# Performance work log

Measured on AMD Instinct MI355X. Metric: run time of the kernel, lower is better.

Reference implementation:

```python
import jax, jax.numpy as jnp
import numpy as np

NUM_ITEM = 2000
DIM_KEY = 256
DIM_VALUE = 128  # number of memory slots
B, T = 256, 512


def setup_inputs() -> dict:
    key = jax.random.key(0)
    ks = jax.random.split(key, 16)
    s = 0.05
    return {
        'item_seq': jax.random.randint(ks[0], (B, T), 0, NUM_ITEM),
        'correct_seq': jax.random.randint(ks[1], (B, T), 0, 2),
        'k_emb': jax.random.normal(ks[2], (NUM_ITEM, DIM_KEY)) * s,
        'v_emb': jax.random.normal(ks[3], (2 * NUM_ITEM, DIM_KEY)) * s,
        'Mk': jax.random.normal(ks[4], (DIM_VALUE, DIM_KEY)) * s,
        'Mv0': jax.random.normal(ks[5], (DIM_VALUE, DIM_KEY)) * s,
        'e_W': jax.random.normal(ks[6], (DIM_KEY, DIM_KEY)) * s,
        'e_b': jnp.zeros((DIM_KEY,)),
        'a_W': jax.random.normal(ks[7], (DIM_KEY, DIM_KEY)) * s,
        'a_b': jnp.zeros((DIM_KEY,)),
        'f_W': jax.random.normal(ks[8], (DIM_KEY, 2 * DIM_KEY)) * s,
        'f_b': jnp.zeros((DIM_KEY,)),
        'p_W': jax.random.normal(ks[9], (1, DIM_KEY)) * s,
        'p_b': jnp.zeros((1,)),
    }


def reference(item_seq, correct_seq, k_emb, v_emb, Mk, Mv0, e_W, e_b, a_W, a_b, f_W, f_b, p_W, p_b):
    num_item = k_emb.shape[0]
    x = item_seq + num_item * correct_seq            # [B, T]
    k = k_emb[item_seq]                              # [B, T, dk]
    v = v_emb[x]                                     # [B, T, dk]
    w = jax.nn.softmax(jnp.einsum('btk,vk->btv', k, Mk), axis=-1)  # [B, T, dv]
    e = jax.nn.sigmoid(v @ e_W.T + e_b)              # erase gate   [B, T, dk]
    a = jnp.tanh(v @ a_W.T + a_b)                    # add vector   [B, T, dk]

    bsz = item_seq.shape[0]
    Mvt0 = jnp.broadcast_to(Mv0[None], (bsz,) + Mv0.shape)  # [B, dv, dk]

    def step(Mvt, inp):
        wt, et, at = inp                              # [B,dv], [B,dk], [B,dk]
        # read uses the memory state BEFORE the update (Mv[:, :-1] in torch)
        read = jnp.einsum('bv,bvk->bk', wt, Mvt)      # [B, dk]
        wt_ = wt[:, :, None]
        Mvt = Mvt * (1.0 - wt_ * et[:, None, :]) + wt_ * at[:, None, :]
        return Mvt, read

    # time-major scan; Mvt stays resident in the carry
    _, reads = jax.lax.scan(
        step, Mvt0,
        (jnp.swapaxes(w, 0, 1), jnp.swapaxes(e, 0, 1), jnp.swapaxes(a, 0, 1)))
    reads = jnp.swapaxes(reads, 0, 1)                 # [B, T, dk]

    f = jnp.tanh(jnp.concatenate([reads, k], axis=-1) @ f_W.T + f_b)  # [B, T, dk]
    # dropout is identity in eval mode
    predict_score = jax.nn.sigmoid(f @ p_W.T + p_b)[..., 0]          # [B, T]
    return predict_score
```

## Files before the change

### kernel.cpp

```cpp
#include <hip/hip_runtime.h>
#include <hip/hip_bf16.h>


#define T_SEQ 512
#define DK    256
#define DV    128
#define NITEM 2000
#define BT    131072

typedef __attribute__((ext_vector_type(8))) short bf16x8;
typedef __attribute__((ext_vector_type(4))) float f32x4;
typedef __attribute__((ext_vector_type(2))) float f32x2;

__device__ __forceinline__ float bf2f(unsigned short u) {
    return __uint_as_float(((unsigned int)u) << 16);
}
__device__ __forceinline__ unsigned short f2bf(float x) {
    unsigned int u = __float_as_uint(x);
    return (unsigned short)((u + 0x7fffu + ((u >> 16) & 1u)) >> 16);
}
__device__ __forceinline__ float fast_rcp(float x) { return __builtin_amdgcn_rcpf(x); }
__device__ __forceinline__ float fast_sigmoid(float x) { return fast_rcp(1.f + __expf(-x)); }
__device__ __forceinline__ float fast_tanh(float x) {
    float t = __expf(2.f * x);
    return (t - 1.f) * fast_rcp(t + 1.f);
}

__device__ __forceinline__ f32x2 pk_fma(f32x2 a, f32x2 b, f32x2 c) {
#if __has_builtin(__builtin_elementwise_fma)
    return __builtin_elementwise_fma(a, b, c);
#else
    f32x2 d; d.x = fmaf(a.x, b.x, c.x); d.y = fmaf(a.y, b.y, c.y); return d;
#endif
}

__global__ __launch_bounds__(256) void k0_cvt(
    const float* __restrict__ s0, const float* __restrict__ s1,
    const float* __restrict__ s2, const float* __restrict__ s3,
    const float* __restrict__ s4,
    unsigned short* __restrict__ d0, unsigned short* __restrict__ d1,
    unsigned short* __restrict__ d2, unsigned short* __restrict__ d3,
    unsigned short* __restrict__ d4,
    int n0, int n1, int n2, int n3, int n4)
{
    const float* s; unsigned short* d; int n;
    switch (blockIdx.y) {
        case 0:  s = s0; d = d0; n = n0; break;
        case 1:  s = s1; d = d1; n = n1; break;
        case 2:  s = s2; d = d2; n = n2; break;
        case 3:  s = s3; d = d3; n = n3; break;
        default: s = s4; d = d4; n = n4; break;
    }
    int i4 = (blockIdx.x * 256 + threadIdx.x) * 4;
    if (i4 < n) {
        float4 v = *(const float4*)(s + i4);
        ushort4 o;
        o.x = f2bf(v.x); o.y = f2bf(v.y); o.z = f2bf(v.z); o.w = f2bf(v.w);
        *(ushort4*)(d + i4) = o;
    }
}

__global__ __launch_bounds__(256) void k1_wea(
    const int* __restrict__ item_seq, const int* __restrict__ correct_seq,
    const unsigned short* __restrict__ k_bf, const unsigned short* __restrict__ v_bf,
    const unsigned short* __restrict__ Mk_bf,
    const unsigned short* __restrict__ eW_bf, const float* __restrict__ e_b,
    const unsigned short* __restrict__ aW_bf, const float* __restrict__ a_b,
    unsigned short* __restrict__ Wout, unsigned short* __restrict__ Eout,
    unsigned short* __restrict__ Aout)
{
    const int m_tile = blockIdx.x;
    const int n_tile = blockIdx.y;
    const int tid  = threadIdx.x;
    const int lane = tid & 63;
    const int wv   = tid >> 6;

    __shared__ int idx_s[128];
    __shared__ unsigned short A_s[128 * 40];
    __shared__ unsigned short B_s[128 * 40];

    const unsigned short* Atab = (n_tile == 0) ? k_bf : v_bf;
    const unsigned short* Wtab; int wrow0;
    if (n_tile == 0)      { Wtab = Mk_bf; wrow0 = 0;   }
    else if (n_tile == 1) { Wtab = eW_bf; wrow0 = 0;   }
    else if (n_tile == 2) { Wtab = eW_bf; wrow0 = 128; }
    else if (n_tile == 3) { Wtab = aW_bf; wrow0 = 0;   }
    else                  { Wtab = aW_bf; wrow0 = 128; }

    if (tid < 128) {
        int pos = m_tile * 128 + tid;
        int it = item_seq[pos];
        int co = correct_seq[pos];
        idx_s[tid] = (n_tile == 0) ? it : (it + NITEM * co);
    }
    __syncthreads();

    int myrow[4], myc4[4], myidx[4];
    #pragma unroll
    for (int j = 0; j < 4; ++j) {
        int chunk = tid + 256 * j;
        myrow[j] = chunk >> 3;
        myc4[j]  = chunk & 7;
        myidx[j] = idx_s[myrow[j]];
    }

    f32x4 acc[2][8];
    #pragma unroll
    for (int mi = 0; mi < 2; ++mi)
        #pragma unroll
        for (int ni = 0; ni < 8; ++ni)
            acc[mi][ni] = (f32x4){0.f, 0.f, 0.f, 0.f};

    for (int bk = 0; bk < 8; ++bk) {
        int k0 = bk * 32;
        #pragma unroll
        for (int j = 0; j < 4; ++j) {
            int row = myrow[j], c4 = myc4[j];
            *(ushort4*)&A_s[row * 40 + c4 * 4] =
                *(const ushort4*)(Atab + (long)myidx[j] * DK + k0 + c4 * 4);
            *(ushort4*)&B_s[row * 40 + c4 * 4] =
                *(const ushort4*)(Wtab + (long)(wrow0 + row) * DK + k0 + c4 * 4);
        }
        __syncthreads();

        const int kq = lane >> 4;
        const int rr = lane & 15;
        bf16x8 af[2], bfr[8];
        #pragma unroll
        for (int mi = 0; mi < 2; ++mi)
            af[mi] = *(const bf16x8*)&A_s[(wv * 32 + mi * 16 + rr) * 40 + kq * 8];
        #pragma unroll
        for (int ni = 0; ni < 8; ++ni)
            bfr[ni] = *(const bf16x8*)&B_s[(ni * 16 + rr) * 40 + kq * 8];
        #pragma unroll
        for (int ni = 0; ni < 8; ++ni)
            #pragma unroll
            for (int mi = 0; mi < 2; ++mi)
                acc[mi][ni] = __builtin_amdgcn_mfma_f32_16x16x32_bf16(
                    af[mi], bfr[ni], acc[mi][ni], 0, 0, 0);
        __syncthreads();
    }

    const int rowbase = m_tile * 128 + wv * 32;
    const int cgrp = lane >> 4;
    const int cc   = lane & 15;

    if (n_tile == 0) {
        #pragma unroll
        for (int mi = 0; mi < 2; ++mi) {
            #pragma unroll
            for (int i = 0; i < 4; ++i) {
                float m = -1e30f;
                #pragma unroll
                for (int ni = 0; ni < 8; ++ni) m = fmaxf(m, acc[mi][ni][i]);
                m = fmaxf(m, __shfl_xor(m, 1));
                m = fmaxf(m, __shfl_xor(m, 2));
                m = fmaxf(m, __shfl_xor(m, 4));
                m = fmaxf(m, __shfl_xor(m, 8));
                float p[8]; float s = 0.f;
                #pragma unroll
                for (int ni = 0; ni < 8; ++ni) { p[ni] = __expf(acc[mi][ni][i] - m); s += p[ni]; }
                s += __shfl_xor(s, 1); s += __shfl_xor(s, 2);
                s += __shfl_xor(s, 4); s += __shfl_xor(s, 8);
                float inv = fast_rcp(s);
                int row = rowbase + mi * 16 + cgrp * 4 + i;
                #pragma unroll
                for (int ni = 0; ni < 8; ++ni)
                    Wout[(long)row * 128 + ni * 16 + cc] = f2bf(p[ni] * inv);
            }
        }
    } else {
        const bool is_e = (n_tile <= 2);
        const float* bias = is_e ? e_b : a_b;
        const int colbase = (is_e ? (n_tile - 1) : (n_tile - 3)) * 128;
        unsigned short* Out = is_e ? Eout : Aout;
        #pragma unroll
        for (int ni = 0; ni < 8; ++ni) {
            int colp = colbase + ni * 16 + cc;
            float bb = bias[colp];
            #pragma unroll
            for (int mi = 0; mi < 2; ++mi) {
                #pragma unroll
                for (int i = 0; i < 4; ++i) {
                    int row = rowbase + mi * 16 + cgrp * 4 + i;
                    float x = acc[mi][ni][i] + bb;
                    float v = is_e ? fast_sigmoid(x) : fast_tanh(x);
                    Out[(long)row * 256 + colp] = f2bf(v);
                }
            }
        }
    }
}

__global__ __launch_bounds__(512, 1) void k2_scan(
    const float* __restrict__ Mv0,
    const unsigned short* __restrict__ Wws, const unsigned short* __restrict__ Ews,
    const unsigned short* __restrict__ Aws, unsigned short* __restrict__ Rws)
{
    const int b   = blockIdx.x;
    const int tid = threadIdx.x;
    const int kq  = tid & 63;
    const int vo  = tid >> 6;

    __shared__ float4 part[8][8][64];

    f32x2 Ma[16], Mb[16];
    #pragma unroll
    for (int j = 0; j < 16; ++j) {
        float4 m4 = *(const float4*)(Mv0 + (vo * 16 + j) * DK + kq * 4);
        Ma[j] = (f32x2){m4.x, m4.y};
        Mb[j] = (f32x2){m4.z, m4.w};
    }

    const long pos0 = (long)b * T_SEQ;
    const unsigned int* Wd = (const unsigned int*)Wws;
    const int wslot = vo * 8 + (kq & 7);

    unsigned int wdA = Wd[(pos0 + 0) * 64 + wslot];
    uint2 edA = *(const uint2*)(Ews + (pos0 + 0) * 256 + kq * 4);
    uint2 adA = *(const uint2*)(Aws + (pos0 + 0) * 256 + kq * 4);
    unsigned int wdB = Wd[(pos0 + 1) * 64 + wslot];
    uint2 edB = *(const uint2*)(Ews + (pos0 + 1) * 256 + kq * 4);
    uint2 adB = *(const uint2*)(Aws + (pos0 + 1) * 256 + kq * 4);

#define K2_STEP(T, SLOT, WD, ED, AD)                                           \
    {                                                                          \
        const unsigned int wd = WD;                                            \
        const uint2 ed = ED, ad = AD;                                          \
        {         \
            long pn = pos0 + ((T) + 2 < T_SEQ ? (T) + 2 : T_SEQ - 1);          \
            WD = Wd[pn * 64 + wslot];                                          \
            ED = *(const uint2*)(Ews + pn * 256 + kq * 4);                     \
            AD = *(const uint2*)(Aws + pn * 256 + kq * 4);                     \
        }                                                                      \
        f32x2 ea = (f32x2){__uint_as_float(ed.x << 16),                        \
                           __uint_as_float(ed.x & 0xffff0000u)};               \
        f32x2 eb = (f32x2){__uint_as_float(ed.y << 16),                        \
                           __uint_as_float(ed.y & 0xffff0000u)};               \
        f32x2 aa = (f32x2){__uint_as_float(ad.x << 16),                        \
                           __uint_as_float(ad.x & 0xffff0000u)};               \
        f32x2 ab = (f32x2){__uint_as_float(ad.y << 16),                        \
                           __uint_as_float(ad.y & 0xffff0000u)};               \
        f32x2 nea = -ea, neb = -eb;                                            \
        f32x2 ra = (f32x2){0.f, 0.f}, rb = (f32x2){0.f, 0.f};                  \
        _Pragma("unroll")                                                      \
        for (int p = 0; p < 8; ++p) {                                          \
            unsigned int d = __builtin_amdgcn_readlane(wd, p);                 \
            float s0 = __uint_as_float(d << 16);                               \
            float s1 = __uint_as_float(d & 0xffff0000u);                       \
            {                                                                  \
                f32x2 s2 = (f32x2){s0, s0};                                    \
                f32x2 ma = Ma[2 * p], mb = Mb[2 * p];                          \
                ra = pk_fma(s2, ma, ra);                                       \
                rb = pk_fma(s2, mb, rb);                                       \
                f32x2 ta = pk_fma(nea, ma, aa);                                \
                f32x2 tb = pk_fma(neb, mb, ab);                                \
                Ma[2 * p] = pk_fma(s2, ta, ma);                                \
                Mb[2 * p] = pk_fma(s2, tb, mb);                                \
            }                                                                  \
            {                                                                  \
                f32x2 s2 = (f32x2){s1, s1};                                    \
                f32x2 ma = Ma[2 * p + 1], mb = Mb[2 * p + 1];                  \
                ra = pk_fma(s2, ma, ra);                                       \
                rb = pk_fma(s2, mb, rb);                                       \
                f32x2 ta = pk_fma(nea, ma, aa);                                \
                f32x2 tb = pk_fma(neb, mb, ab);                                \
                Ma[2 * p + 1] = pk_fma(s2, ta, ma);                            \
                Mb[2 * p + 1] = pk_fma(s2, tb, mb);                            \
            }                                                                  \
        }                                                                      \
        part[SLOT][vo][kq] = float4{ra.x, ra.y, rb.x, rb.y};                   \
    }

    for (int tc = 0; tc < T_SEQ; tc += 8) {
        K2_STEP(tc + 0, 0, wdA, edA, adA)
        K2_STEP(tc + 1, 1, wdB, edB, adB)
        K2_STEP(tc + 2, 2, wdA, edA, adA)
        K2_STEP(tc + 3, 3, wdB, edB, adB)
        K2_STEP(tc + 4, 4, wdA, edA, adA)
        K2_STEP(tc + 5, 5, wdB, edB, adB)
        K2_STEP(tc + 6, 6, wdA, edA, adA)
        K2_STEP(tc + 7, 7, wdB, edB, adB)
        __syncthreads();
        {
            float4 s = part[vo][0][kq];
            #pragma unroll
            for (int w2 = 1; w2 < 8; ++w2) {
                float4 r = part[vo][w2][kq];
                s.x += r.x; s.y += r.y; s.z += r.z; s.w += r.w;
            }
            ushort4 o;
            o.x = f2bf(s.x); o.y = f2bf(s.y); o.z = f2bf(s.z); o.w = f2bf(s.w);
            *(ushort4*)(Rws + (pos0 + tc + vo) * 256 + kq * 4) = o;
        }
        __syncthreads();
    }
#undef K2_STEP
}

__global__ __launch_bounds__(256) void k3_f(
    const int* __restrict__ item_seq,
    const unsigned short* __restrict__ k_bf,
    const unsigned short* __restrict__ fW_bf, const float* __restrict__ f_b,
    const unsigned short* __restrict__ Rws,
    unsigned short* __restrict__ Fout)
{
    const int m_tile = blockIdx.x;
    const int nt  = blockIdx.y;
    const int tid = threadIdx.x;
    const int lane = tid & 63;
    const int wv   = tid >> 6;

    __shared__ int idx_s[128];
    __shared__ unsigned short A_s[128 * 40];
    __shared__ unsigned short B_s[128 * 40];

    if (tid < 128) idx_s[tid] = item_seq[m_tile * 128 + tid];
    __syncthreads();

    int myrow[4], myc4[4], myidx[4];
    #pragma unroll
    for (int j = 0; j < 4; ++j) {
        int chunk = tid + 256 * j;
        myrow[j] = chunk >> 3;
        myc4[j]  = chunk & 7;
        myidx[j] = idx_s[myrow[j]];
    }

    f32x4 acc[2][8];
    #pragma unroll
    for (int mi = 0; mi < 2; ++mi)
        #pragma unroll
        for (int ni = 0; ni < 8; ++ni)
            acc[mi][ni] = (f32x4){0.f, 0.f, 0.f, 0.f};

    for (int bk = 0; bk < 16; ++bk) {
        int k0 = bk * 32;
        #pragma unroll
        for (int j = 0; j < 4; ++j) {
            int row = myrow[j], c4 = myc4[j];
            ushort4 ap;
            if (k0 < 256) {
                long pos = (long)m_tile * 128 + row;
                ap = *(const ushort4*)(Rws + pos * 256 + k0 + c4 * 4);
            } else {
                ap = *(const ushort4*)(k_bf + (long)myidx[j] * DK + (k0 - 256) + c4 * 4);
            }
            *(ushort4*)&A_s[row * 40 + c4 * 4] = ap;
            *(ushort4*)&B_s[row * 40 + c4 * 4] =
                *(const ushort4*)(fW_bf + (long)(nt * 128 + row) * 512 + k0 + c4 * 4);
        }
        __syncthreads();

        const int kq = lane >> 4;
        const int rr = lane & 15;
        bf16x8 af[2], bfr[8];
        #pragma unroll
        for (int mi = 0; mi < 2; ++mi)
            af[mi] = *(const bf16x8*)&A_s[(wv * 32 + mi * 16 + rr) * 40 + kq * 8];
        #pragma unroll
        for (int ni = 0; ni < 8; ++ni)
            bfr[ni] = *(const bf16x8*)&B_s[(ni * 16 + rr) * 40 + kq * 8];
        #pragma unroll
        for (int ni = 0; ni < 8; ++ni)
            #pragma unroll
            for (int mi = 0; mi < 2; ++mi)
                acc[mi][ni] = __builtin_amdgcn_mfma_f32_16x16x32_bf16(
                    af[mi], bfr[ni], acc[mi][ni], 0, 0, 0);
        __syncthreads();
    }

    const int rowbase = m_tile * 128 + wv * 32;
    const int cgrp = lane >> 4;
    const int cc   = lane & 15;
    #pragma unroll
    for (int ni = 0; ni < 8; ++ni) {
        int colp = nt * 128 + ni * 16 + cc;
        float bb = f_b[colp];
        #pragma unroll
        for (int mi = 0; mi < 2; ++mi) {
            #pragma unroll
            for (int i = 0; i < 4; ++i) {
                int row = rowbase + mi * 16 + cgrp * 4 + i;
                Fout[(long)row * 256 + colp] = f2bf(fast_tanh(acc[mi][ni][i] + bb));
            }
        }
    }
}

__global__ __launch_bounds__(256) void k4_pred(
    const unsigned short* __restrict__ Fws,
    const float* __restrict__ p_W, const float* __restrict__ p_b,
    float* __restrict__ out)
{
    const int tid  = threadIdx.x;
    const int lane = tid & 63;
    const int wgid = blockIdx.x * 4 + (tid >> 6);
    const float4 pw = *(const float4*)(p_W + lane * 4);
    const float pb = p_b[0];
    #pragma unroll 4
    for (int r = 0; r < 64; ++r) {
        long row = (long)wgid * 64 + r;
        ushort4 q = *(const ushort4*)(Fws + row * 256 + lane * 4);
        float partial = bf2f(q.x) * pw.x + bf2f(q.y) * pw.y
                      + bf2f(q.z) * pw.z + bf2f(q.w) * pw.w;
        #pragma unroll
        for (int off = 32; off >= 1; off >>= 1) partial += __shfl_xor(partial, off);
        if (lane == 0) out[row] = fast_sigmoid(partial + pb);
    }
}

extern "C" void kernel_launch(void* const* d_in, const int* in_sizes, int n_in,
                              void* d_out, int out_size, void* d_ws, size_t ws_size,
                              hipStream_t stream)
{
    const int*   item_seq    = (const int*)d_in[0];
    const int*   correct_seq = (const int*)d_in[1];
    const float* k_emb = (const float*)d_in[2];
    const float* v_emb = (const float*)d_in[3];
    const float* Mk    = (const float*)d_in[4];
    const float* Mv0   = (const float*)d_in[5];
    const float* e_W   = (const float*)d_in[6];
    const float* e_b   = (const float*)d_in[7];
    const float* a_W   = (const float*)d_in[8];
    const float* a_b   = (const float*)d_in[9];
    const float* f_W   = (const float*)d_in[10];
    const float* f_b   = (const float*)d_in[11];
    const float* p_W   = (const float*)d_in[12];
    const float* p_b   = (const float*)d_in[13];
    float* out = (float*)d_out;

    char* ws = (char*)d_ws;
    unsigned short* Wws = (unsigned short*)(ws);
    unsigned short* Ews = (unsigned short*)(ws + 33554432ll);
    unsigned short* Aws = (unsigned short*)(ws + 100663296ll);
    unsigned short* Rws = (unsigned short*)(ws + 167772160ll);

    unsigned short* kA_bf = Rws;
    unsigned short* v_bf  = Rws + 512000;
    unsigned short* Mk_bf = Rws + 1536000;
    unsigned short* eW_bf = Rws + 1568768;
    unsigned short* aW_bf = Rws + 1634304;
    unsigned short* k3_bf = Wws;
    unsigned short* fW_bf = Wws + 512000;

    k0_cvt<<<dim3(1000, 5), dim3(256), 0, stream>>>(
        k_emb, v_emb, Mk, e_W, a_W,
        kA_bf, v_bf, Mk_bf, eW_bf, aW_bf,
        512000, 1024000, 32768, 65536, 65536);

    k1_wea<<<dim3(1024, 5), dim3(256), 0, stream>>>(
        item_seq, correct_seq, kA_bf, v_bf, Mk_bf, eW_bf, e_b, aW_bf, a_b,
        Wws, Ews, Aws);

    k2_scan<<<dim3(256), dim3(512), 0, stream>>>(Mv0, Wws, Ews, Aws, Rws);

    k0_cvt<<<dim3(500, 2), dim3(256), 0, stream>>>(
        k_emb, f_W, nullptr, nullptr, nullptr,
        k3_bf, fW_bf, nullptr, nullptr, nullptr,
        512000, 131072, 0, 0, 0);

    k3_f<<<dim3(1024, 2), dim3(256), 0, stream>>>(
        item_seq, k3_bf, fW_bf, f_b, Rws, Ews );

    k4_pred<<<dim3(512), dim3(256), 0, stream>>>(Ews, p_W, p_b, out);
}
```

Baseline: 518.6 us.

## Split scan over key dimension into two blocks per batch row

The recurrent memory scan now launches two blocks per batch element, each owning half of the 256-wide key dimension, so each thread holds 16 f32x2 memory values instead of 32. This doubles the number of independent blocks for the serial time loop (512 blocks on a 256-CU device instead of 256) and lets more waves be resident. The cost is duplicated loads of the attention weights per block and smaller per-thread work relative to the per-step sync and reduction overhead.

New measurement: 533.5 us. 1.03x slower.

```diff
diff --git a/kernel.cpp b/kernel.cpp
--- a/kernel.cpp
+++ b/kernel.cpp
@@ -192,57 +192,56 @@
     }
 }
 
-__global__ __launch_bounds__(512, 1) void k2_scan(
+__global__ __launch_bounds__(512, 4) void k2_scan(
     const float* __restrict__ Mv0,
     const unsigned short* __restrict__ Wws, const unsigned short* __restrict__ Ews,
     const unsigned short* __restrict__ Aws, unsigned short* __restrict__ Rws)
 {
-    const int b   = blockIdx.x;
+    const int b   = blockIdx.x >> 1;
+    const int kh  = blockIdx.x & 1;
     const int tid = threadIdx.x;
     const int kq  = tid & 63;
     const int vo  = tid >> 6;
 
-    __shared__ float4 part[8][8][64];
-
-    f32x2 Ma[16], Mb[16];
+    __shared__ f32x2 part[8][8][64];
+
+    f32x2 M[16];
     #pragma unroll
     for (int j = 0; j < 16; ++j) {
-        float4 m4 = *(const float4*)(Mv0 + (vo * 16 + j) * DK + kq * 4);
-        Ma[j] = (f32x2){m4.x, m4.y};
-        Mb[j] = (f32x2){m4.z, m4.w};
+        float2 m2 = *(const float2*)(Mv0 + (vo * 16 + j) * DK + kh * 128 + kq * 2);
+        M[j] = (f32x2){m2.x, m2.y};
     }
 
     const long pos0 = (long)b * T_SEQ;
     const unsigned int* Wd = (const unsigned int*)Wws;
+    const unsigned int* Ed = (const unsigned int*)Ews;
+    const unsigned int* Ad = (const unsigned int*)Aws;
     const int wslot = vo * 8 + (kq & 7);
+    const int eslot = kh * 64 + kq;
 
     unsigned int wdA = Wd[(pos0 + 0) * 64 + wslot];
-    uint2 edA = *(const uint2*)(Ews + (pos0 + 0) * 256 + kq * 4);
-    uint2 adA = *(const uint2*)(Aws + (pos0 + 0) * 256 + kq * 4);
+    unsigned int edA = Ed[(pos0 + 0) * 128 + eslot];
+    unsigned int adA = Ad[(pos0 + 0) * 128 + eslot];
     unsigned int wdB = Wd[(pos0 + 1) * 64 + wslot];
-    uint2 edB = *(const uint2*)(Ews + (pos0 + 1) * 256 + kq * 4);
-    uint2 adB = *(const uint2*)(Aws + (pos0 + 1) * 256 + kq * 4);
+    unsigned int edB = Ed[(pos0 + 1) * 128 + eslot];
+    unsigned int adB = Ad[(pos0 + 1) * 128 + eslot];
 
 #define K2_STEP(T, SLOT, WD, ED, AD)                                           \
     {                                                                          \
         const unsigned int wd = WD;                                            \
-        const uint2 ed = ED, ad = AD;                                          \
+        const unsigned int ed = ED, ad = AD;                                   \
         {         \
             long pn = pos0 + ((T) + 2 < T_SEQ ? (T) + 2 : T_SEQ - 1);          \
             WD = Wd[pn * 64 + wslot];                                          \
-            ED = *(const uint2*)(Ews + pn * 256 + kq * 4);                     \
-            AD = *(const uint2*)(Aws + pn * 256 + kq * 4);                     \
+            ED = Ed[pn * 128 + eslot];                                         \
+            AD = Ad[pn * 128 + eslot];                                         \
         }                                                                      \
-        f32x2 ea = (f32x2){__uint_as_float(ed.x << 16),                        \
-                           __uint_as_float(ed.x & 0xffff0000u)};               \
-        f32x2 eb = (f32x2){__uint_as_float(ed.y << 16),                        \
-                           __uint_as_float(ed.y & 0xffff0000u)};               \
-        f32x2 aa = (f32x2){__uint_as_float(ad.x << 16),                        \
-                           __uint_as_float(ad.x & 0xffff0000u)};               \
-        f32x2 ab = (f32x2){__uint_as_float(ad.y << 16),                        \
-                           __uint_as_float(ad.y & 0xffff0000u)};               \
-        f32x2 nea = -ea, neb = -eb;                                            \
-        f32x2 ra = (f32x2){0.f, 0.f}, rb = (f32x2){0.f, 0.f};                  \
+        f32x2 ea = (f32x2){__uint_as_float(ed << 16),                          \
+                           __uint_as_float(ed & 0xffff0000u)};                 \
+        f32x2 aa = (f32x2){__uint_as_float(ad << 16),                          \
+                           __uint_as_float(ad & 0xffff0000u)};                 \
+        f32x2 nea = -ea;                                                       \
+        f32x2 r = (f32x2){0.f, 0.f};                                           \
         _Pragma("unroll")                                                      \
         for (int p = 0; p < 8; ++p) {                                          \
             unsigned int d = __builtin_amdgcn_readlane(wd, p);                 \
@@ -250,26 +249,20 @@
             float s1 = __uint_as_float(d & 0xffff0000u);                       \
             {                                                                  \
                 f32x2 s2 = (f32x2){s0, s0};                                    \
-                f32x2 ma = Ma[2 * p], mb = Mb[2 * p];                          \
-                ra = pk_fma(s2, ma, ra);                                       \
-                rb = pk_fma(s2, mb, rb);                                       \
-                f32x2 ta = pk_fma(nea, ma, aa);                                \
-                f32x2 tb = pk_fma(neb, mb, ab);                                \
-                Ma[2 * p] = pk_fma(s2, ta, ma);                                \
-                Mb[2 * p] = pk_fma(s2, tb, mb);                                \
+                f32x2 m = M[2 * p];                                            \
+                r = pk_fma(s2, m, r);                  \
+                f32x2 t2 = pk_fma(nea, m, aa);                    \
+                M[2 * p] = pk_fma(s2, t2, m);             \
             }                                                                  \
             {                                                                  \
                 f32x2 s2 = (f32x2){s1, s1};                                    \
-                f32x2 ma = Ma[2 * p + 1], mb = Mb[2 * p + 1];                  \
-                ra = pk_fma(s2, ma, ra);                                       \
-                rb = pk_fma(s2, mb, rb);                                       \
-                f32x2 ta = pk_fma(nea, ma, aa);                                \
-                f32x2 tb = pk_fma(neb, mb, ab);                                \
-                Ma[2 * p + 1] = pk_fma(s2, ta, ma);                            \
-                Mb[2 * p + 1] = pk_fma(s2, tb, mb);                            \
+                f32x2 m = M[2 * p + 1];                                        \
+                r = pk_fma(s2, m, r);                                          \
+                f32x2 t2 = pk_fma(nea, m, aa);                                 \
+                M[2 * p + 1] = pk_fma(s2, t2, m);                              \
             }                                                                  \
         }                                                                      \
-        part[SLOT][vo][kq] = float4{ra.x, ra.y, rb.x, rb.y};                   \
+        part[SLOT][vo][kq] = r;                                                \
     }
 
     for (int tc = 0; tc < T_SEQ; tc += 8) {
@@ -283,15 +276,15 @@
         K2_STEP(tc + 7, 7, wdB, edB, adB)
         __syncthreads();
         {
-            float4 s = part[vo][0][kq];
+            f32x2 s = part[vo][0][kq];
             #pragma unroll
             for (int w2 = 1; w2 < 8; ++w2) {
-                float4 r = part[vo][w2][kq];
-                s.x += r.x; s.y += r.y; s.z += r.z; s.w += r.w;
+                f32x2 r = part[vo][w2][kq];
+                s.x += r.x; s.y += r.y;
             }
-            ushort4 o;
-            o.x = f2bf(s.x); o.y = f2bf(s.y); o.z = f2bf(s.z); o.w = f2bf(s.w);
-            *(ushort4*)(Rws + (pos0 + tc + vo) * 256 + kq * 4) = o;
+            ushort2 o;
+            o.x = f2bf(s.x); o.y = f2bf(s.y);
+            *(ushort2*)(Rws + (pos0 + tc + vo) * 256 + kh * 128 + kq * 2) = o;
         }
         __syncthreads();
     }
@@ -453,7 +446,7 @@
         item_seq, correct_seq, kA_bf, v_bf, Mk_bf, eW_bf, e_b, aW_bf, a_b,
         Wws, Ews, Aws);
 
-    k2_scan<<<dim3(256), dim3(512), 0, stream>>>(Mv0, Wws, Ews, Aws, Rws);
+    k2_scan<<<dim3(512), dim3(512), 0, stream>>>(Mv0, Wws, Ews, Aws, Rws);
 
     k0_cvt<<<dim3(500, 2), dim3(256), 0, stream>>>(
         k_emb, f_W, nullptr, nullptr, nullptr,
```

## Store scan memory state in packed fp16 and use fdot2 for reads

Applied to the files above, without the earlier changes.

Converts the W/E/A workspaces from bf16 to fp16 and keeps the per-batch memory matrix in registers as packed half2 pairs across adjacent memory slots. The read is computed with the fdot2 instruction and the erase/add update with packed fp16 FMAs, which halves register use and roughly halves the ALU work per step. Prefetch depth grows from two to four steps, and launch bounds now allow more blocks per CU. The cost is accuracy: the recurrent state accumulates in fp16 over 512 steps, so rounding error can build up.

Measured after the change: 483.6 us. -6.7%, faster.

```diff
diff --git a/kernel.cpp b/kernel.cpp
--- a/kernel.cpp
+++ b/kernel.cpp
@@ -1,5 +1,6 @@
 #include <hip/hip_runtime.h>
 #include <hip/hip_bf16.h>
+#include <hip/hip_fp16.h>
 
 
 #define T_SEQ 512
@@ -10,7 +11,8 @@
 
 typedef __attribute__((ext_vector_type(8))) short bf16x8;
 typedef __attribute__((ext_vector_type(4))) float f32x4;
-typedef __attribute__((ext_vector_type(2))) float f32x2;
+typedef _Float16 h16x2 __attribute__((ext_vector_type(2)));
+typedef _Float16 h16x4 __attribute__((ext_vector_type(4)));
 
 __device__ __forceinline__ float bf2f(unsigned short u) {
     return __uint_as_float(((unsigned int)u) << 16);
@@ -18,6 +20,10 @@
 __device__ __forceinline__ unsigned short f2bf(float x) {
     unsigned int u = __float_as_uint(x);
     return (unsigned short)((u + 0x7fffu + ((u >> 16) & 1u)) >> 16);
+}
+__device__ __forceinline__ unsigned short f2h(float x) {
+    _Float16 h = (_Float16)x;
+    return __builtin_bit_cast(unsigned short, h);
 }
 __device__ __forceinline__ float fast_rcp(float x) { return __builtin_amdgcn_rcpf(x); }
 __device__ __forceinline__ float fast_sigmoid(float x) { return fast_rcp(1.f + __expf(-x)); }
@@ -26,11 +32,18 @@
     return (t - 1.f) * fast_rcp(t + 1.f);
 }
 
-__device__ __forceinline__ f32x2 pk_fma(f32x2 a, f32x2 b, f32x2 c) {
+__device__ __forceinline__ float fdot2_(h16x2 a, h16x2 b, float c) {
+#if __has_builtin(__builtin_amdgcn_fdot2)
+    return __builtin_amdgcn_fdot2(a, b, c, false);
+#else
+    return (float)a[0] * (float)b[0] + (float)a[1] * (float)b[1] + c;
+#endif
+}
+__device__ __forceinline__ h16x2 pkfma(h16x2 a, h16x2 b, h16x2 c) {
 #if __has_builtin(__builtin_elementwise_fma)
     return __builtin_elementwise_fma(a, b, c);
 #else
-    f32x2 d; d.x = fmaf(a.x, b.x, c.x); d.y = fmaf(a.y, b.y, c.y); return d;
+    return a * b + c;
 #endif
 }
 
@@ -166,7 +179,7 @@
                 int row = rowbase + mi * 16 + cgrp * 4 + i;
                 #pragma unroll
                 for (int ni = 0; ni < 8; ++ni)
-                    Wout[(long)row * 128 + ni * 16 + cc] = f2bf(p[ni] * inv);
+                    Wout[(long)row * 128 + ni * 16 + cc] = f2h(p[ni] * inv);
             }
         }
     } else {
@@ -185,14 +198,14 @@
                     int row = rowbase + mi * 16 + cgrp * 4 + i;
                     float x = acc[mi][ni][i] + bb;
                     float v = is_e ? fast_sigmoid(x) : fast_tanh(x);
-                    Out[(long)row * 256 + colp] = f2bf(v);
+                    Out[(long)row * 256 + colp] = f2h(v);
                 }
             }
         }
     }
 }
 
-__global__ __launch_bounds__(512, 1) void k2_scan(
+__global__ __launch_bounds__(512, 4) void k2_scan(
     const float* __restrict__ Mv0,
     const unsigned short* __restrict__ Wws, const unsigned short* __restrict__ Ews,
     const unsigned short* __restrict__ Aws, unsigned short* __restrict__ Rws)
@@ -204,83 +217,78 @@
 
     __shared__ float4 part[8][8][64];
 
-    f32x2 Ma[16], Mb[16];
-    #pragma unroll
-    for (int j = 0; j < 16; ++j) {
-        float4 m4 = *(const float4*)(Mv0 + (vo * 16 + j) * DK + kq * 4);
-        Ma[j] = (f32x2){m4.x, m4.y};
-        Mb[j] = (f32x2){m4.z, m4.w};
+    h16x2 M[4][8];
+    #pragma unroll
+    for (int p = 0; p < 8; ++p) {
+        const float4 r0 = *(const float4*)(Mv0 + (vo * 16 + 2 * p) * DK + kq * 4);
+        const float4 r1 = *(const float4*)(Mv0 + (vo * 16 + 2 * p + 1) * DK + kq * 4);
+        M[0][p] = (h16x2){(_Float16)r0.x, (_Float16)r1.x};
+        M[1][p] = (h16x2){(_Float16)r0.y, (_Float16)r1.y};
+        M[2][p] = (h16x2){(_Float16)r0.z, (_Float16)r1.z};
+        M[3][p] = (h16x2){(_Float16)r0.w, (_Float16)r1.w};
     }
 
     const long pos0 = (long)b * T_SEQ;
     const unsigned int* Wd = (const unsigned int*)Wws;
     const int wslot = vo * 8 + (kq & 7);
 
-    unsigned int wdA = Wd[(pos0 + 0) * 64 + wslot];
-    uint2 edA = *(const uint2*)(Ews + (pos0 + 0) * 256 + kq * 4);
-    uint2 adA = *(const uint2*)(Aws + (pos0 + 0) * 256 + kq * 4);
-    unsigned int wdB = Wd[(pos0 + 1) * 64 + wslot];
-    uint2 edB = *(const uint2*)(Ews + (pos0 + 1) * 256 + kq * 4);
-    uint2 adB = *(const uint2*)(Aws + (pos0 + 1) * 256 + kq * 4);
+    unsigned int wdA, wdB, wdC, wdD;
+    uint2 edA, edB, edC, edD, adA, adB, adC, adD;
+    wdA = Wd[(pos0 + 0) * 64 + wslot];
+    edA = *(const uint2*)(Ews + (pos0 + 0) * 256 + kq * 4);
+    adA = *(const uint2*)(Aws + (pos0 + 0) * 256 + kq * 4);
+    wdB = Wd[(pos0 + 1) * 64 + wslot];
+    edB = *(const uint2*)(Ews + (pos0 + 1) * 256 + kq * 4);
+    adB = *(const uint2*)(Aws + (pos0 + 1) * 256 + kq * 4);
+    wdC = Wd[(pos0 + 2) * 64 + wslot];
+    edC = *(const uint2*)(Ews + (pos0 + 2) * 256 + kq * 4);
+    adC = *(const uint2*)(Aws + (pos0 + 2) * 256 + kq * 4);
+    wdD = Wd[(pos0 + 3) * 64 + wslot];
+    edD = *(const uint2*)(Ews + (pos0 + 3) * 256 + kq * 4);
+    adD = *(const uint2*)(Aws + (pos0 + 3) * 256 + kq * 4);
 
 #define K2_STEP(T, SLOT, WD, ED, AD)                                           \
     {                                                                          \
         const unsigned int wd = WD;                                            \
         const uint2 ed = ED, ad = AD;                                          \
-        {         \
-            long pn = pos0 + ((T) + 2 < T_SEQ ? (T) + 2 : T_SEQ - 1);          \
+        {                     \
+            long pn = pos0 + ((T) + 4 < T_SEQ ? (T) + 4 : T_SEQ - 1);          \
             WD = Wd[pn * 64 + wslot];                                          \
             ED = *(const uint2*)(Ews + pn * 256 + kq * 4);                     \
             AD = *(const uint2*)(Aws + pn * 256 + kq * 4);                     \
         }                                                                      \
-        f32x2 ea = (f32x2){__uint_as_float(ed.x << 16),                        \
-                           __uint_as_float(ed.x & 0xffff0000u)};               \
-        f32x2 eb = (f32x2){__uint_as_float(ed.y << 16),                        \
-                           __uint_as_float(ed.y & 0xffff0000u)};               \
-        f32x2 aa = (f32x2){__uint_as_float(ad.x << 16),                        \
-                           __uint_as_float(ad.x & 0xffff0000u)};               \
-        f32x2 ab = (f32x2){__uint_as_float(ad.y << 16),                        \
-                           __uint_as_float(ad.y & 0xffff0000u)};               \
-        f32x2 nea = -ea, neb = -eb;                                            \
-        f32x2 ra = (f32x2){0.f, 0.f}, rb = (f32x2){0.f, 0.f};                  \
+        const h16x4 ev = __builtin_bit_cast(h16x4, ed);                        \
+        const h16x4 av = __builtin_bit_cast(h16x4, ad);                        \
+        const h16x2 es0 = (h16x2){ev[0], ev[0]}, as0 = (h16x2){av[0], av[0]};  \
+        const h16x2 es1 = (h16x2){ev[1], ev[1]}, as1 = (h16x2){av[1], av[1]};  \
+        const h16x2 es2 = (h16x2){ev[2], ev[2]}, as2 = (h16x2){av[2], av[2]};  \
+        const h16x2 es3 = (h16x2){ev[3], ev[3]}, as3 = (h16x2){av[3], av[3]};  \
+        float r0 = 0.f, r1 = 0.f, r2 = 0.f, r3 = 0.f;                          \
         _Pragma("unroll")                                                      \
         for (int p = 0; p < 8; ++p) {                                          \
-            unsigned int d = __builtin_amdgcn_readlane(wd, p);                 \
-            float s0 = __uint_as_float(d << 16);                               \
-            float s1 = __uint_as_float(d & 0xffff0000u);                       \
-            {                                                                  \
-                f32x2 s2 = (f32x2){s0, s0};                                    \
-                f32x2 ma = Ma[2 * p], mb = Mb[2 * p];                          \
-                ra = pk_fma(s2, ma, ra);                                       \
-                rb = pk_fma(s2, mb, rb);                                       \
-                f32x2 ta = pk_fma(nea, ma, aa);                                \
-                f32x2 tb = pk_fma(neb, mb, ab);                                \
-                Ma[2 * p] = pk_fma(s2, ta, ma);                                \
-                Mb[2 * p] = pk_fma(s2, tb, mb);                                \
-            }                                                                  \
-            {                                                                  \
-                f32x2 s2 = (f32x2){s1, s1};                                    \
-                f32x2 ma = Ma[2 * p + 1], mb = Mb[2 * p + 1];                  \
-                ra = pk_fma(s2, ma, ra);                                       \
-                rb = pk_fma(s2, mb, rb);                                       \
-                f32x2 ta = pk_fma(nea, ma, aa);                                \
-                f32x2 tb = pk_fma(neb, mb, ab);                                \
-                Ma[2 * p + 1] = pk_fma(s2, ta, ma);                            \
-                Mb[2 * p + 1] = pk_fma(s2, tb, mb);                            \
-            }                                                                  \
+            const h16x2 wpk = __builtin_bit_cast(h16x2,                        \
+                __builtin_amdgcn_readlane(wd, p));                             \
+            r0 = fdot2_(wpk, M[0][p], r0);             \
+            r1 = fdot2_(wpk, M[1][p], r1);                                     \
+            r2 = fdot2_(wpk, M[2][p], r2);                                     \
+            r3 = fdot2_(wpk, M[3][p], r3);                                     \
+            M[0][p] = pkfma(wpk, pkfma(-es0, M[0][p], as0), M[0][p]);          \
+            M[1][p] = pkfma(wpk, pkfma(-es1, M[1][p], as1), M[1][p]);          \
+            M[2][p] = pkfma(wpk, pkfma(-es2, M[2][p], as2), M[2][p]);          \
+            M[3][p] = pkfma(wpk, pkfma(-es3, M[3][p], as3), M[3][p]);          \
         }                                                                      \
-        part[SLOT][vo][kq] = float4{ra.x, ra.y, rb.x, rb.y};                   \
+        part[SLOT][vo][kq] = float4{r0, r1, r2, r3};                           \
     }
 
     for (int tc = 0; tc < T_SEQ; tc += 8) {
         K2_STEP(tc + 0, 0, wdA, edA, adA)
         K2_STEP(tc + 1, 1, wdB, edB, adB)
-        K2_STEP(tc + 2, 2, wdA, edA, adA)
-        K2_STEP(tc + 3, 3, wdB, edB, adB)
+        K2_STEP(tc + 2, 2, wdC, edC, adC)
+        K2_STEP(tc + 3, 3, wdD, edD, adD)
         K2_STEP(tc + 4, 4, wdA, edA, adA)
         K2_STEP(tc + 5, 5, wdB, edB, adB)
-        K2_STEP(tc + 6, 6, wdA, edA, adA)
-        K2_STEP(tc + 7, 7, wdB, edB, adB)
+        K2_STEP(tc + 6, 6, wdC, edC, adC)
+        K2_STEP(tc + 7, 7, wdD, edD, adD)
         __syncthreads();
         {
             float4 s = part[vo][0][kq];
```
